# Optimization experiments

Measured on AMD Instinct MI355X. Metric: run time of the kernel, lower is better.

Reference implementation:

```python
import jax, jax.numpy as jnp
import numpy as np

N = 30000; F = 16; E = 300000
HD = 256; NH = 8; C = HD // NH; L = 3
S = 256; K = 128
NH_CA = 4; HDC = HD // NH_CA


def _ln(x, g, b):
    mu = jnp.mean(x, -1, keepdims=True)
    v = jnp.mean((x - mu) ** 2, -1, keepdims=True)
    return (x - mu) / jnp.sqrt(v + 1e-5) * g + b


def setup_inputs() -> dict:
    ks = iter(jax.random.split(jax.random.key(0), 64))
    def nrm(sh, s=0.05):
        return jax.random.normal(next(ks), sh, jnp.float32) * s
    def zeros(sh):
        return jnp.zeros(sh, jnp.float32)
    def ones(sh):
        return jnp.ones(sh, jnp.float32)
    inp = {}
    inp['x'] = jax.random.normal(next(ks), (N, F), jnp.float32)
    inp['edge_index'] = jax.random.randint(next(ks), (2, E), 0, N, jnp.int32)
    inp['batch'] = jnp.zeros((N,), jnp.int32)
    inp['sheet_node_idx'] = jax.random.randint(next(ks), (S, K), 0, N, jnp.int32)
    inp['sheet_features'] = jax.random.normal(next(ks), (S, F), jnp.float32)
    # pre_transform
    inp['pre_W'] = nrm((F, HD)); inp['pre_b'] = zeros((HD,))
    # stacked GATv2 layers (lin_l, lin_r, att, bias)
    inp['gat_Wl'] = nrm((L, HD, HD)); inp['gat_Wr'] = nrm((L, HD, HD))
    inp['gat_att'] = nrm((L, NH, C)); inp['gat_b'] = zeros((L, HD))
    # geometry encoder
    inp['geo_W1'] = nrm((F, HD)); inp['geo_b1'] = zeros((HD,))
    inp['geo_g1'] = ones((HD,)); inp['geo_be1'] = zeros((HD,))
    inp['geo_W2'] = nrm((HD, HD)); inp['geo_b2'] = zeros((HD,))
    inp['geo_g2'] = ones((HD,)); inp['geo_be2'] = zeros((HD,))
    # cross attention (4 heads)
    inp['ca_Wq'] = nrm((HD, HD)); inp['ca_bq'] = zeros((HD,))
    inp['ca_Wk'] = nrm((HD, HD)); inp['ca_bk'] = zeros((HD,))
    inp['ca_Wv'] = nrm((HD, HD)); inp['ca_bv'] = zeros((HD,))
    inp['ca_Wo'] = nrm((HD, HD)); inp['ca_bo'] = zeros((HD,))
    # q_mlp
    inp['q_W1'] = nrm((2 * HD, HD)); inp['q_b1'] = zeros((HD,))
    inp['q_g1'] = ones((HD,)); inp['q_be1'] = zeros((HD,))
    inp['q_W2'] = nrm((HD, HD // 2)); inp['q_b2'] = zeros((HD // 2,))
    inp['q_g2'] = ones((HD // 2,)); inp['q_be2'] = zeros((HD // 2,))
    inp['q_W3'] = nrm((HD // 2, 1)); inp['q_b3'] = zeros((1,))
    # state_done_predictor
    inp['d_W1'] = nrm((HD, HD // 2)); inp['d_b1'] = zeros((HD // 2,))
    inp['d_g1'] = ones((HD // 2,)); inp['d_be1'] = zeros((HD // 2,))
    inp['d_W2'] = nrm((HD // 2, 1)); inp['d_b2'] = zeros((1,))
    return inp


def _fwd(x, sheet_features, pre_W, pre_b, gat_Wl, gat_Wr, gat_att, gat_b,
         geo_W1, geo_b1, geo_g1, geo_be1, geo_W2, geo_b2, geo_g2, geo_be2,
         ca_Wq, ca_bq, ca_Wk, ca_bk, ca_Wv, ca_bv, ca_Wo, ca_bo,
         q_W1, q_b1, q_g1, q_be1, q_W2, q_b2, q_g2, q_be2, q_W3, q_b3,
         d_W1, d_b1, d_g1, d_be1, d_W2, d_b2,
         edge_index, batch, sheet_node_idx):
    loops = jnp.arange(N, dtype=edge_index.dtype)  # PyG GATv2Conv add_self_loops=True
    src = jnp.concatenate([edge_index[0], loops])
    dst = jnp.concatenate([edge_index[1], loops])
    h = x @ pre_W + pre_b  # [N, HD]
    for l in range(L):
        xl = (h @ gat_Wl[l]).reshape(N, NH, C)  # source messages
        xr = (h @ gat_Wr[l]).reshape(N, NH, C)  # target
        m = jax.nn.leaky_relu(xl[src] + xr[dst], 0.2)  # [E+N, NH, C]
        e = jnp.einsum('ehc,hc->eh', m, gat_att[l])
        emax = jax.ops.segment_max(e, dst, num_segments=N)
        a = jnp.exp(e - emax[dst])
        denom = jax.ops.segment_sum(a, dst, num_segments=N)
        alpha = a / (denom[dst] + 1e-16)  # scatter softmax over incoming edges
        h = jax.ops.segment_sum(alpha[:, :, None] * xl[src], dst, num_segments=N)
        h = jax.nn.elu(h.reshape(N, HD) + gat_b[l])
    cnt = jax.ops.segment_sum(jnp.ones((N,), h.dtype), batch, num_segments=1)
    g = jax.ops.segment_sum(h, batch, num_segments=1) / cnt[:, None]  # [1, HD]
    sheet = h[sheet_node_idx].mean(axis=1)  # [S, HD] per-sheet gather+mean
    geo = jax.nn.relu(_ln(sheet_features @ geo_W1 + geo_b1, geo_g1, geo_be1))
    geo = jax.nn.relu(_ln(geo @ geo_W2 + geo_b2, geo_g2, geo_be2))
    qh = (sheet @ ca_Wq + ca_bq).reshape(S, NH_CA, HDC)
    kh = (geo @ ca_Wk + ca_bk).reshape(S, NH_CA, HDC)
    vh = (geo @ ca_Wv + ca_bv).reshape(S, NH_CA, HDC)
    att = jax.nn.softmax(jnp.einsum('qhd,khd->hqk', qh, kh) / jnp.sqrt(jnp.float32(HDC)), axis=-1)
    fused = jnp.einsum('hqk,khd->qhd', att, vh).reshape(S, HD) @ ca_Wo + ca_bo
    hq = jnp.concatenate([fused, jnp.broadcast_to(g, (S, HD))], axis=1)  # [S, 2*HD]
    hq = jax.nn.relu(_ln(hq @ q_W1 + q_b1, q_g1, q_be1))
    hq = jax.nn.relu(_ln(hq @ q_W2 + q_b2, q_g2, q_be2))
    q_values = (hq @ q_W3 + q_b3)[:, 0]  # [S]
    hd = jax.nn.relu(_ln(g @ d_W1 + d_b1, d_g1, d_be1))
    done_logit = (hd @ d_W2 + d_b2)[:, 0]  # [1]
    return q_values, done_logit


def reference(x, edge_index, batch, sheet_node_idx, sheet_features, pre_W, pre_b,
              gat_Wl, gat_Wr, gat_att, gat_b,
              geo_W1, geo_b1, geo_g1, geo_be1, geo_W2, geo_b2, geo_g2, geo_be2,
              ca_Wq, ca_bq, ca_Wk, ca_bk, ca_Wv, ca_bv, ca_Wo, ca_bo,
              q_W1, q_b1, q_g1, q_be1, q_W2, q_b2, q_g2, q_be2, q_W3, q_b3,
              d_W1, d_b1, d_g1, d_be1, d_W2, d_b2):
    return _fwd(x, sheet_features, pre_W, pre_b, gat_Wl, gat_Wr, gat_att, gat_b,
                geo_W1, geo_b1, geo_g1, geo_be1, geo_W2, geo_b2, geo_g2, geo_be2,
                ca_Wq, ca_bq, ca_Wk, ca_bk, ca_Wv, ca_bv, ca_Wo, ca_bo,
                q_W1, q_b1, q_g1, q_be1, q_W2, q_b2, q_g2, q_be2, q_W3, q_b3,
                d_W1, d_b1, d_g1, d_be1, d_W2, d_b2,
                edge_index, batch, sheet_node_idx)
```

## Files before the change

### kernel.cpp

```cpp
#include <hip/hip_runtime.h>
#include <hip/hip_bf16.h>
#include <stdint.h>

#define NN 30000
#define MPAD 30080
#define FI 16
#define EE 300000
#define ETOT (EE + NN)
#define HD 256
#define NH 8
#define CH 32
#define NL 3
#define SS 256
#define KS 128
#define NHC 4
#define HC 64
#define GSB 256
#define RPB 118
#define SCB 118

typedef _Float16 half8 __attribute__((ext_vector_type(8)));
typedef _Float16 half4v __attribute__((ext_vector_type(4)));
typedef _Float16 half2v __attribute__((ext_vector_type(2)));
typedef float f32x4 __attribute__((ext_vector_type(4)));

__device__ __forceinline__ float wsum(float v) {
#pragma unroll
  for (int d = 1; d < 64; d <<= 1) v += __shfl_xor(v, d);
  return v;
}

__device__ __forceinline__ half2v h2max(half2v a, half2v b) {
#if __has_builtin(__builtin_elementwise_max)
  return __builtin_elementwise_max(a, b);
#else
  half2v r; r[0] = a[0] > b[0] ? a[0] : b[0]; r[1] = a[1] > b[1] ? a[1] : b[1];
  return r;
#endif
}

__device__ __forceinline__ float h2dot(half2v a, half2v b, float c) {
#if __has_builtin(__builtin_amdgcn_fdot2)
  return __builtin_amdgcn_fdot2(a, b, c, false);
#else
  return c + (float)a[0] * (float)b[0] + (float)a[1] * (float)b[1];
#endif
}

__device__ __forceinline__ float ln_fast(float a, int t, int n, float* red16,
    const float* __restrict__ G, const float* __restrict__ Be, bool relu)
{
  float av = (t < n) ? a : 0.f;
  float s = wsum(av), s2 = wsum(av * av);
  if ((t & 63) == 0) { red16[t >> 6] = s; red16[8 + (t >> 6)] = s2; }
  __syncthreads();
  float sum = red16[0] + red16[1] + red16[2] + red16[3];
  float sq  = red16[8] + red16[9] + red16[10] + red16[11];
  float mu = sum / n;
  float var = sq / n - mu * mu;
  float o = 0.f;
  if (t < n) {
    o = (a - mu) * rsqrtf(var + 1e-5f) * G[t] + Be[t];
    if (relu) o = fmaxf(o, 0.f);
  }
  __syncthreads();
  return o;
}

__global__ __launch_bounds__(256) void k_init(int* __restrict__ cnt,
    int* __restrict__ gcnt, _Float16* __restrict__ h16pad)
{
  int i = blockIdx.x * 256 + threadIdx.x;
  if (i < NN) cnt[i] = 0;
  if (i == 0) gcnt[0] = 0;
  if (i < (MPAD - NN) * HD) h16pad[i] = (_Float16)0.f;
}

__global__ __launch_bounds__(256) void k_wconv(const float* __restrict__ Wl,
    const float* __restrict__ Wr, _Float16* __restrict__ WT)
{
  int m = blockIdx.x >> 8;
  int n = blockIdx.x & 255;
  int k = threadIdx.x;
  int l = m >> 1;
  const float* W = (m & 1) ? (Wr + (size_t)l * HD * HD) : (Wl + (size_t)l * HD * HD);
  WT[((size_t)m * HD + n) * HD + k] = (_Float16)W[k * HD + n];
}

__global__ __launch_bounds__(256) void k_wconvT(
    const float* __restrict__ geo_W2, const float* __restrict__ ca_Wq,
    const float* __restrict__ ca_Wk, const float* __restrict__ ca_Wv,
    const float* __restrict__ ca_Wo, const float* __restrict__ q_W1,
    const float* __restrict__ q_W2,
    _Float16* __restrict__ Tgeo2, _Float16* __restrict__ Tq,
    _Float16* __restrict__ Tk, _Float16* __restrict__ Tv,
    _Float16* __restrict__ To, _Float16* __restrict__ Tq1,
    _Float16* __restrict__ Tq2)
{
  int b = blockIdx.x, t = threadIdx.x;
  if (b < 1280) {
    int seg = b >> 8;
    int n = b & 255;
    const float* src = (seg == 0) ? geo_W2 : (seg == 1) ? ca_Wq : (seg == 2) ? ca_Wk
                     : (seg == 3) ? ca_Wv : ca_Wo;
    _Float16* dst = (seg == 0) ? Tgeo2 : (seg == 1) ? Tq : (seg == 2) ? Tk
                  : (seg == 3) ? Tv : To;
    dst[(size_t)n * 256 + t] = (_Float16)src[(size_t)t * 256 + n];
  } else if (b < 1536) {
    int n = b - 1280;
    Tq1[(size_t)n * 512 + t]       = (_Float16)q_W1[(size_t)t * 256 + n];
    Tq1[(size_t)n * 512 + 256 + t] = (_Float16)q_W1[(size_t)(256 + t) * 256 + n];
  } else {
    int n = b - 1536;
    Tq2[(size_t)n * 256 + t] = (_Float16)q_W2[(size_t)t * 128 + n];
  }
}

__global__ __launch_bounds__(256) void k_pre(const float* __restrict__ x,
    const float* __restrict__ W, const float* __restrict__ b,
    _Float16* __restrict__ H16)
{
  __shared__ float Ws[FI][HD];
  __shared__ float xs[8][FI];
  int r0 = blockIdx.x * 8;
  int t = threadIdx.x;
  for (int i = t; i < FI * HD; i += 256) Ws[i >> 8][i & 255] = W[i];
  if (t < 8 * FI) xs[t >> 4][t & 15] = x[(size_t)(r0 + (t >> 4)) * FI + (t & 15)];
  __syncthreads();
  float bj = b[t];
  for (int r = 0; r < 8; ++r) {
    float acc = bj;
#pragma unroll
    for (int k = 0; k < FI; ++k) acc += xs[r][k] * Ws[k][t];
    H16[(size_t)(r0 + r) * HD + t] = (_Float16)acc;
  }
}

__global__ __launch_bounds__(256) void k_count(const int* __restrict__ ei, int* __restrict__ cnt)
{
  int i = blockIdx.x * 256 + threadIdx.x;
  if (i >= ETOT) return;
  int dst = (i < EE) ? ei[EE + i] : (i - EE);
  atomicAdd(&cnt[dst], 1);
}

__global__ __launch_bounds__(256) void k_scanA(const int* __restrict__ cnt,
    int* __restrict__ rowptr, int* __restrict__ btot)
{
  __shared__ int wt[4];
  int b = blockIdx.x, t = threadIdx.x;
  int i = b * 256 + t;
  int v = (i < NN) ? cnt[i] : 0;
  int lane = t & 63, w = t >> 6;
  int s = v;
#pragma unroll
  for (int d = 1; d < 64; d <<= 1) {
    int u = __shfl_up(s, d);
    if (lane >= d) s += u;
  }
  if (lane == 63) wt[w] = s;
  __syncthreads();
  int off = 0;
  for (int k = 0; k < w; ++k) off += wt[k];
  if (i < NN) rowptr[i] = off + s - v;
  if (t == 255) btot[b] = off + s;
}

__global__ __launch_bounds__(128) void k_scanB(const int* __restrict__ btot,
    int* __restrict__ boff, int* __restrict__ rowptr)
{
  __shared__ int wt[2];
  int t = threadIdx.x;
  int v = (t < SCB) ? btot[t] : 0;
  int lane = t & 63, w = t >> 6;
  int s = v;
#pragma unroll
  for (int d = 1; d < 64; d <<= 1) {
    int u = __shfl_up(s, d);
    if (lane >= d) s += u;
  }
  if (lane == 63) wt[w] = s;
  __syncthreads();
  int off = (w == 1) ? wt[0] : 0;
  if (t < SCB) boff[t] = off + s - v;
  if (t == 127) rowptr[NN] = wt[0] + wt[1];
}

__global__ __launch_bounds__(256) void k_scanC(int* __restrict__ rowptr,
    const int* __restrict__ boff, int* __restrict__ wptr)
{
  int b = blockIdx.x, t = threadIdx.x;
  int i = b * 256 + t;
  if (i < NN) {
    int r = rowptr[i] + boff[b];
    rowptr[i] = r;
    wptr[i] = r;
  }
}

__global__ __launch_bounds__(256) void k_scatter(const int* __restrict__ ei,
    int* __restrict__ wptr, int* __restrict__ csr_src)
{
  int i = blockIdx.x * 256 + threadIdx.x;
  if (i >= ETOT) return;
  int src = (i < EE) ? ei[i] : (i - EE);
  int dst = (i < EE) ? ei[EE + i] : (i - EE);
  int pos = atomicAdd(&wptr[dst], 1);
  csr_src[pos] = src;
}

#define BK 64
__global__ __launch_bounds__(256) void k_gemm16(const _Float16* __restrict__ A,
    const _Float16* __restrict__ WT,
    _Float16* __restrict__ Xl, _Float16* __restrict__ Xr)
{
  __shared__ __align__(16) _Float16 As[128 * BK];
  __shared__ __align__(16) _Float16 Bs[128 * BK];
  int t = threadIdx.x;
  int w = t >> 6, lane = t & 63;
  int row0 = blockIdx.x * 128;
  int ct = blockIdx.y;
  const _Float16* Bmat = WT + (size_t)(ct >> 1) * HD * HD + (size_t)(ct & 1) * 128 * HD;
  _Float16* Out = (ct >> 1) ? Xr : Xl;
  int j0 = (ct & 1) * 128;

  f32x4 acc[4][4] = {};
  int wr = w >> 1, wc = w & 1;

  for (int k0 = 0; k0 < HD; k0 += BK) {
#pragma unroll
    for (int i = 0; i < 4; ++i) {
      int p = (i * 4 + w) * 64 + lane;
      int row = p >> 3, s = p & 7;
      int g = s ^ (row & 7);
      const _Float16* srcA = A + (size_t)(row0 + row) * HD + k0 + g * 8;
      __builtin_amdgcn_global_load_lds(
        (const __attribute__((address_space(1))) void*)srcA,
        (__attribute__((address_space(3))) void*)((char*)As + (i * 4 + w) * 1024),
        16, 0, 0);
      const _Float16* srcB = Bmat + (size_t)row * HD + k0 + g * 8;
      __builtin_amdgcn_global_load_lds(
        (const __attribute__((address_space(1))) void*)srcB,
        (__attribute__((address_space(3))) void*)((char*)Bs + (i * 4 + w) * 1024),
        16, 0, 0);
    }
    __syncthreads();
#pragma unroll
    for (int ks = 0; ks < 2; ++ks) {
      half8 af[4], bfr[4];
      int kslot = ks * 4 + (lane >> 4);
#pragma unroll
      for (int mi = 0; mi < 4; ++mi) {
        int rl = wr * 64 + mi * 16 + (lane & 15);
        int ps = kslot ^ (rl & 7);
        af[mi] = *(const half8*)((const char*)As + rl * 128 + ps * 16);
      }
#pragma unroll
      for (int ni = 0; ni < 4; ++ni) {
        int nl = wc * 64 + ni * 16 + (lane & 15);
        int ps = kslot ^ (nl & 7);
        bfr[ni] = *(const half8*)((const char*)Bs + nl * 128 + ps * 16);
      }
#pragma unroll
      for (int mi = 0; mi < 4; ++mi)
#pragma unroll
        for (int ni = 0; ni < 4; ++ni)
          acc[mi][ni] = __builtin_amdgcn_mfma_f32_16x16x32_f16(af[mi], bfr[ni], acc[mi][ni], 0, 0, 0);
    }
    __syncthreads();
  }
  int crow = (lane >> 4) * 4;
  int ccol = lane & 15;
#pragma unroll
  for (int mi = 0; mi < 4; ++mi)
#pragma unroll
    for (int ni = 0; ni < 4; ++ni) {
      size_t base_r = row0 + wr * 64 + mi * 16 + crow;
      int c = j0 + wc * 64 + ni * 16 + ccol;
#pragma unroll
      for (int r = 0; r < 4; ++r)
        Out[(base_r + r) * HD + c] = (_Float16)acc[mi][ni][r];
    }
}

__global__ __launch_bounds__(256) void k_edgeagg(const _Float16* __restrict__ Xl,
    const _Float16* __restrict__ Xr, const float* __restrict__ attw,
    const float* __restrict__ bias, const int* __restrict__ rowptr,
    const int* __restrict__ csr_src, _Float16* __restrict__ H16)
{
  int node = blockIdx.x * 4 + (threadIdx.x >> 6);
  int lane = threadIdx.x & 63;
  if (node >= NN) return;
  int st = rowptr[node], en = rowptr[node + 1];
  int c = lane * 4;
  half4v xrv = *(const half4v*)(Xr + (size_t)node * HD + c);
  half2v r01; r01[0] = xrv[0]; r01[1] = xrv[1];
  half2v r23; r23[0] = xrv[2]; r23[1] = xrv[3];
  float4 wvf = *(const float4*)(attw + c);
  half2v w01; w01[0] = (_Float16)wvf.x; w01[1] = (_Float16)wvf.y;
  half2v w23; w23[0] = (_Float16)wvf.z; w23[1] = (_Float16)wvf.w;
  half2v c02; c02[0] = (_Float16)0.2f; c02[1] = (_Float16)0.2f;

  float mh = -1e30f, dsum = 0.f;
  float a0 = 0.f, a1 = 0.f, a2 = 0.f, a3 = 0.f;

  half4v vx[4];
#pragma unroll
  for (int k = 0; k < 4; ++k) {
    int ii = st + k; if (ii >= en) ii = en - 1;
    vx[k] = *(const half4v*)(Xl + (size_t)csr_src[ii] * HD + c);
  }

  for (int i = st; i < en; i += 4) {
    half4v nvx[4];
#pragma unroll
    for (int k = 0; k < 4; ++k) {
      int ii = i + 4 + k; ii = (ii < en) ? ii : (en - 1);
      nvx[k] = *(const half4v*)(Xl + (size_t)csr_src[ii] * HD + c);
    }
    float e[4];
#pragma unroll
    for (int k = 0; k < 4; ++k) {
      half2v x01; x01[0] = vx[k][0]; x01[1] = vx[k][1];
      half2v x23; x23[0] = vx[k][2]; x23[1] = vx[k][3];
      half2v s0 = x01 + r01;
      half2v s1 = x23 + r23;
      half2v m0 = h2max(s0, s0 * c02);
      half2v m1 = h2max(s1, s1 * c02);
      float ek = h2dot(m1, w23, h2dot(m0, w01, 0.f));
      ek += __shfl_xor(ek, 1);
      ek += __shfl_xor(ek, 2);
      ek += __shfl_xor(ek, 4);
      e[k] = (i + k < en) ? ek : -1e30f;
    }
    float pmax = fmaxf(fmaxf(e[0], e[1]), fmaxf(e[2], e[3]));
    if (__any(pmax > mh + 8.f)) {
      float nm = fmaxf(mh, pmax);
      float sc = __expf(mh - nm);
      a0 *= sc; a1 *= sc; a2 *= sc; a3 *= sc; dsum *= sc;
      mh = nm;
    }
    float ps = 0.f;
#pragma unroll
    for (int k = 0; k < 4; ++k) {
      float pw = __expf(e[k] - mh);
      a0 += pw * (float)vx[k][0];
      a1 += pw * (float)vx[k][1];
      a2 += pw * (float)vx[k][2];
      a3 += pw * (float)vx[k][3];
      ps += pw;
    }
    dsum += ps;
#pragma unroll
    for (int k = 0; k < 4; ++k) vx[k] = nvx[k];
  }
  float inv = 1.f / (dsum + 1e-16f);
  float4 bb = *(const float4*)(bias + c);
  float o0 = a0 * inv + bb.x, o1 = a1 * inv + bb.y;
  float o2 = a2 * inv + bb.z, o3 = a3 * inv + bb.w;
  o0 = (o0 > 0.f) ? o0 : expm1f(o0);
  o1 = (o1 > 0.f) ? o1 : expm1f(o1);
  o2 = (o2 > 0.f) ? o2 : expm1f(o2);
  o3 = (o3 > 0.f) ? o3 : expm1f(o3);
  half4v h4;
  h4[0] = (_Float16)o0; h4[1] = (_Float16)o1; h4[2] = (_Float16)o2; h4[3] = (_Float16)o3;
  *(half4v*)(H16 + (size_t)node * HD + c) = h4;
}

__global__ __launch_bounds__(256) void k_gsum(const _Float16* __restrict__ H,
    const int* __restrict__ batch, float* __restrict__ gpart, int* __restrict__ gcnt)
{
  __shared__ float flagf[RPB];
  __shared__ int scount;
  int b = blockIdx.x, t = threadIdx.x;
  int r0 = b * RPB;
  int nr = NN - r0; if (nr > RPB) nr = RPB; if (nr < 0) nr = 0;
  if (t == 0) scount = 0;
  __syncthreads();
  if (t < nr) {
    int ok = (batch[r0 + t] == 0) ? 1 : 0;
    flagf[t] = (float)ok;
    if (ok) atomicAdd(&scount, 1);
  }
  __syncthreads();
  float a0 = 0.f, a1 = 0.f, a2 = 0.f, a3 = 0.f;
  const _Float16* Hp = H + (size_t)r0 * HD + t;
  int r = 0;
  for (; r + 4 <= nr; r += 4) {
    float v0 = (float)Hp[(size_t)(r + 0) * HD];
    float v1 = (float)Hp[(size_t)(r + 1) * HD];
    float v2 = (float)Hp[(size_t)(r + 2) * HD];
    float v3 = (float)Hp[(size_t)(r + 3) * HD];
    a0 += v0 * flagf[r + 0]; a1 += v1 * flagf[r + 1];
    a2 += v2 * flagf[r + 2]; a3 += v3 * flagf[r + 3];
  }
  for (; r < nr; ++r) a0 += (float)Hp[(size_t)r * HD] * flagf[r];
  gpart[(size_t)b * HD + t] = (a0 + a1) + (a2 + a3);
  if (t == 0 && scount) atomicAdd(gcnt, scount);
}

__global__ __launch_bounds__(256) void k_gfin(const float* __restrict__ gpart,
    const int* __restrict__ gcnt, float* __restrict__ gvec)
{
  int t = threadIdx.x;
  float a0 = 0.f, a1 = 0.f, a2 = 0.f, a3 = 0.f;
  for (int b = 0; b < GSB; b += 4) {
    a0 += gpart[(size_t)b * HD + t];
    a1 += gpart[(size_t)(b + 1) * HD + t];
    a2 += gpart[(size_t)(b + 2) * HD + t];
    a3 += gpart[(size_t)(b + 3) * HD + t];
  }
  gvec[t] = ((a0 + a1) + (a2 + a3)) / (float)(*gcnt);
}

__global__ __launch_bounds__(256) void k_tail1(const _Float16* __restrict__ h16,
    const int* __restrict__ sheet_idx, const float* __restrict__ sheet_feat,
    const float* __restrict__ geo_W1, const float* __restrict__ geo_b1,
    const float* __restrict__ geo_g1, const float* __restrict__ geo_be1,
    _Float16* __restrict__ sh16, _Float16* __restrict__ g116)
{
  __shared__ float xf[FI];
  __shared__ int sidx[KS];
  __shared__ float red16[16];
  int s = blockIdx.x, t = threadIdx.x;

  if (t < KS) sidx[t] = sheet_idx[s * KS + t];
  if (t >= 240) xf[t - 240] = sheet_feat[s * FI + (t - 240)];
  __syncthreads();

  float pa[8] = {};
#pragma unroll 2
  for (int r = 0; r < KS; r += 8) {
#pragma unroll
    for (int u = 0; u < 8; ++u)
      pa[u] += (float)h16[(size_t)sidx[r + u] * HD + t];
  }
  float shv = ((pa[0] + pa[1]) + (pa[2] + pa[3]) + (pa[4] + pa[5]) + (pa[6] + pa[7])) * (1.f / KS);
  sh16[(size_t)s * HD + t] = (_Float16)shv;

  float a = geo_b1[t];
#pragma unroll
  for (int k = 0; k < FI; ++k) a += xf[k] * geo_W1[k * HD + t];
  float g1 = ln_fast(a, t, 256, red16, geo_g1, geo_be1, true);
  g116[(size_t)s * HD + t] = (_Float16)g1;
}

template <int KD, int NW>
__global__ __launch_bounds__(NW * 64) void k_stageLN(
    const _Float16* __restrict__ X, const _Float16* __restrict__ WT,
    const float* __restrict__ b, const float* __restrict__ G,
    const float* __restrict__ Be, _Float16* __restrict__ Y,
    const float* __restrict__ W3, const float* __restrict__ b3,
    float* __restrict__ outq)
{
  __shared__ float ps[NW * 16], ps2[NW * 16], pq[NW * 16];
  const int NCOL = NW * 64;
  int t = threadIdx.x;
  int w = t >> 6, lane = t & 63;
  int arow = lane & 15, kg = lane >> 4;
  int m0 = blockIdx.x * 16;
  int col0 = w * 64;

  f32x4 acc[4] = {};
#pragma unroll
  for (int ks = 0; ks < KD / 32; ++ks) {
    half8 af = *(const half8*)(X + (size_t)(m0 + arow) * KD + ks * 32 + kg * 8);
#pragma unroll
    for (int n = 0; n < 4; ++n) {
      half8 bf = *(const half8*)(WT + (size_t)(col0 + n * 16 + arow) * KD + ks * 32 + kg * 8);
      acc[n] = __builtin_amdgcn_mfma_f32_16x16x32_f16(af, bf, acc[n], 0, 0, 0);
    }
  }
#pragma unroll
  for (int n = 0; n < 4; ++n) {
    float bv = b[col0 + n * 16 + arow];
#pragma unroll
    for (int r = 0; r < 4; ++r) acc[n][r] += bv;
  }
  float s[4] = {}, s2[4] = {};
#pragma unroll
  for (int n = 0; n < 4; ++n)
#pragma unroll
    for (int r = 0; r < 4; ++r) { float v = acc[n][r]; s[r] += v; s2[r] += v * v; }
#pragma unroll
  for (int d = 1; d < 16; d <<= 1)
#pragma unroll
    for (int r = 0; r < 4; ++r) { s[r] += __shfl_xor(s[r], d); s2[r] += __shfl_xor(s2[r], d); }
  if (arow == 0) {
#pragma unroll
    for (int r = 0; r < 4; ++r) {
      ps[w * 16 + kg * 4 + r] = s[r];
      ps2[w * 16 + kg * 4 + r] = s2[r];
    }
  }
  __syncthreads();
  float mu[4], rs[4];
#pragma unroll
  for (int r = 0; r < 4; ++r) {
    float S = 0.f, S2 = 0.f;
#pragma unroll
    for (int w2 = 0; w2 < NW; ++w2) { S += ps[w2 * 16 + kg * 4 + r]; S2 += ps2[w2 * 16 + kg * 4 + r]; }
    float m = S / NCOL;
    float var = S2 / NCOL - m * m;
    mu[r] = m; rs[r] = rsqrtf(var + 1e-5f);
  }
#pragma unroll
  for (int n = 0; n < 4; ++n) {
    int col = col0 + n * 16 + arow;
    float gv = G[col], bev = Be[col];
#pragma unroll
    for (int r = 0; r < 4; ++r)
      acc[n][r] = fmaxf((acc[n][r] - mu[r]) * rs[r] * gv + bev, 0.f);
  }
  if (Y) {
#pragma unroll
    for (int n = 0; n < 4; ++n) {
      int col = col0 + n * 16 + arow;
#pragma unroll
      for (int r = 0; r < 4; ++r)
        Y[(size_t)(m0 + kg * 4 + r) * NCOL + col] = (_Float16)acc[n][r];
    }
  }
  if (outq) {
    float p[4] = {};
#pragma unroll
    for (int n = 0; n < 4; ++n) {
      float w3 = W3[col0 + n * 16 + arow];
#pragma unroll
      for (int r = 0; r < 4; ++r) p[r] += acc[n][r] * w3;
    }
#pragma unroll
    for (int d = 1; d < 16; d <<= 1)
#pragma unroll
      for (int r = 0; r < 4; ++r) p[r] += __shfl_xor(p[r], d);
    if (arow == 0)
#pragma unroll
      for (int r = 0; r < 4; ++r) pq[w * 16 + kg * 4 + r] = p[r];
    __syncthreads();
    if (w == 0 && arow == 0) {
#pragma unroll
      for (int r = 0; r < 4; ++r) {
        float o = b3[0];
#pragma unroll
        for (int w2 = 0; w2 < NW; ++w2) o += pq[w2 * 16 + kg * 4 + r];
        outq[m0 + kg * 4 + r] = o;
      }
    }
  }
}

__global__ __launch_bounds__(64) void k_qkv(
    const _Float16* __restrict__ sh16, const _Float16* __restrict__ g216,
    const _Float16* __restrict__ Tq, const _Float16* __restrict__ Tk,
    const _Float16* __restrict__ Tv,
    const float* __restrict__ bq, const float* __restrict__ bk,
    const float* __restrict__ bv,
    _Float16* __restrict__ qb, _Float16* __restrict__ kb, _Float16* __restrict__ vb)
{
  int lane = threadIdx.x;
  int arow = lane & 15, kg = lane >> 4;
  int m0 = blockIdx.x * 16;
  int col0 = blockIdx.y * 64;
  int mat = blockIdx.z;
  const _Float16* X = (mat == 0) ? sh16 : g216;
  const _Float16* WT = (mat == 0) ? Tq : (mat == 1) ? Tk : Tv;
  const float* b = (mat == 0) ? bq : (mat == 1) ? bk : bv;
  _Float16* Y = (mat == 0) ? qb : (mat == 1) ? kb : vb;

  f32x4 acc[4] = {};
#pragma unroll
  for (int ks = 0; ks < 8; ++ks) {
    half8 af = *(const half8*)(X + (size_t)(m0 + arow) * 256 + ks * 32 + kg * 8);
#pragma unroll
    for (int n = 0; n < 4; ++n) {
      half8 bf = *(const half8*)(WT + (size_t)(col0 + n * 16 + arow) * 256 + ks * 32 + kg * 8);
      acc[n] = __builtin_amdgcn_mfma_f32_16x16x32_f16(af, bf, acc[n], 0, 0, 0);
    }
  }
#pragma unroll
  for (int n = 0; n < 4; ++n) {
    int col = col0 + n * 16 + arow;
    float bv2 = b[col];
#pragma unroll
    for (int r = 0; r < 4; ++r)
      Y[(size_t)(m0 + kg * 4 + r) * 256 + col] = (_Float16)(acc[n][r] + bv2);
  }
}

__global__ __launch_bounds__(64) void k_wo(
    const _Float16* __restrict__ pv16, const _Float16* __restrict__ To,
    const float* __restrict__ bo, const float* __restrict__ gvec,
    _Float16* __restrict__ hqin)
{
  int lane = threadIdx.x;
  int arow = lane & 15, kg = lane >> 4;
  int m0 = blockIdx.x * 16;
  int col0 = blockIdx.y * 64;

  f32x4 acc[4] = {};
#pragma unroll
  for (int ks = 0; ks < 8; ++ks) {
    half8 af = *(const half8*)(pv16 + (size_t)(m0 + arow) * 256 + ks * 32 + kg * 8);
#pragma unroll
    for (int n = 0; n < 4; ++n) {
      half8 bf = *(const half8*)(To + (size_t)(col0 + n * 16 + arow) * 256 + ks * 32 + kg * 8);
      acc[n] = __builtin_amdgcn_mfma_f32_16x16x32_f16(af, bf, acc[n], 0, 0, 0);
    }
  }
#pragma unroll
  for (int n = 0; n < 4; ++n) {
    int col = col0 + n * 16 + arow;
    float bv = bo[col];
    _Float16 gg = (_Float16)gvec[col];
#pragma unroll
    for (int r = 0; r < 4; ++r) {
      hqin[(size_t)(m0 + kg * 4 + r) * 512 + col] = (_Float16)(acc[n][r] + bv);
      hqin[(size_t)(m0 + kg * 4 + r) * 512 + 256 + col] = gg;
    }
  }
}

__global__ __launch_bounds__(1024) void k_attn(const _Float16* __restrict__ qb,
    const _Float16* __restrict__ kb, const _Float16* __restrict__ vb,
    _Float16* __restrict__ pv16)
{
  __shared__ float qv[HD];
  __shared__ float att[1024];
  __shared__ float red4[1024];
  __shared__ float redm[16];
  __shared__ float reds[16];
  int row = blockIdx.x, t = threadIdx.x;
  int w = t >> 6;

  if (t < 256) qv[t] = (float)qb[(size_t)row * HD + t];
  __syncthreads();

  int h = t >> 8, key = t & 255;
  float e = 0.f;
  {
    const half8* kr = (const half8*)(kb + (size_t)key * HD + h * HC);
    const float* qh = qv + h * HC;
#pragma unroll
    for (int d = 0; d < 8; ++d) {
      half8 kk = kr[d];
#pragma unroll
      for (int u = 0; u < 8; ++u) e += qh[d * 8 + u] * (float)kk[u];
    }
    e *= 0.125f;
  }
  float wm = e;
#pragma unroll
  for (int d = 1; d < 64; d <<= 1) wm = fmaxf(wm, __shfl_xor(wm, d));
  if ((t & 63) == 0) redm[w] = wm;
  __syncthreads();
  float mx = fmaxf(fmaxf(redm[4 * h], redm[4 * h + 1]), fmaxf(redm[4 * h + 2], redm[4 * h + 3]));
  float pw = __expf(e - mx);
  float ws = wsum(pw);
  if ((t & 63) == 0) reds[w] = ws;
  att[t] = pw;
  __syncthreads();

  int kq = t >> 8, j = t & 255;
  int hj = j >> 6;
  float p = 0.f;
  const float* arow = att + hj * 256 + kq * 64;
  const _Float16* vcol = vb + (size_t)(kq * 64) * HD + j;
  for (int k = 0; k < 64; ++k)
    p += arow[k] * (float)vcol[(size_t)k * HD];
  red4[t] = p;
  __syncthreads();
  if (t < 256) {
    int hh = t >> 6;
    float dsum = reds[4 * hh] + reds[4 * hh + 1] + reds[4 * hh + 2] + reds[4 * hh + 3];
    float pv = (red4[t] + red4[256 + t] + red4[512 + t] + red4[768 + t]) / dsum;
    pv16[(size_t)row * HD + t] = (_Float16)pv;
  }
}

__global__ __launch_bounds__(256) void k_done(const float* __restrict__ gvec,
    const float* __restrict__ W1, const float* __restrict__ b1,
    const float* __restrict__ g1, const float* __restrict__ be1,
    const float* __restrict__ W2, const float* __restrict__ b2,
    float* __restrict__ out)
{
  __shared__ float gl[256];
  __shared__ float redc[256];
  __shared__ float red16[16];
  int t = threadIdx.x;
  gl[t] = gvec[t];
  __syncthreads();
  int j2 = t & 127, half = t >> 7;
  float p = 0.f;
#pragma unroll 8
  for (int k = half * 128; k < half * 128 + 128; ++k) p += gl[k] * W1[(size_t)k * 128 + j2];
  redc[t] = p;
  __syncthreads();
  float a = 0.f;
  if (t < 128) a = b1[t] + redc[t] + redc[128 + t];
  float hd = ln_fast(a, t, 128, red16, g1, be1, true);
  float vterm = (t < 128) ? hd * W2[t] : 0.f;
  float ss = wsum(vterm);
  if ((t & 63) == 0) red16[t >> 6] = ss;
  __syncthreads();
  if (t == 0) out[0] = red16[0] + red16[1] + red16[2] + red16[3] + b2[0];
}

extern "C" void kernel_launch(void* const* d_in, const int* in_sizes, int n_in,
                              void* d_out, int out_size, void* d_ws, size_t ws_size,
                              hipStream_t stream) {
  const float* x      = (const float*)d_in[0];
  const int*   ei     = (const int*)d_in[1];
  const int*   batch  = (const int*)d_in[2];
  const int*   sheet_idx = (const int*)d_in[3];
  const float* sheet_feat = (const float*)d_in[4];
  const float* pre_W  = (const float*)d_in[5];
  const float* pre_b  = (const float*)d_in[6];
  const float* gat_Wl = (const float*)d_in[7];
  const float* gat_Wr = (const float*)d_in[8];
  const float* gat_att = (const float*)d_in[9];
  const float* gat_b  = (const float*)d_in[10];
  const float* geo_W1 = (const float*)d_in[11];
  const float* geo_b1 = (const float*)d_in[12];
  const float* geo_g1 = (const float*)d_in[13];
  const float* geo_be1 = (const float*)d_in[14];
  const float* geo_W2 = (const float*)d_in[15];
  const float* geo_b2 = (const float*)d_in[16];
  const float* geo_g2 = (const float*)d_in[17];
  const float* geo_be2 = (const float*)d_in[18];
  const float* ca_Wq = (const float*)d_in[19];
  const float* ca_bq = (const float*)d_in[20];
  const float* ca_Wk = (const float*)d_in[21];
  const float* ca_bk = (const float*)d_in[22];
  const float* ca_Wv = (const float*)d_in[23];
  const float* ca_bv = (const float*)d_in[24];
  const float* ca_Wo = (const float*)d_in[25];
  const float* ca_bo = (const float*)d_in[26];
  const float* q_W1 = (const float*)d_in[27];
  const float* q_b1 = (const float*)d_in[28];
  const float* q_g1 = (const float*)d_in[29];
  const float* q_be1 = (const float*)d_in[30];
  const float* q_W2 = (const float*)d_in[31];
  const float* q_b2 = (const float*)d_in[32];
  const float* q_g2 = (const float*)d_in[33];
  const float* q_be2 = (const float*)d_in[34];
  const float* q_W3 = (const float*)d_in[35];
  const float* q_b3 = (const float*)d_in[36];
  const float* d_W1 = (const float*)d_in[37];
  const float* d_b1 = (const float*)d_in[38];
  const float* d_g1 = (const float*)d_in[39];
  const float* d_be1 = (const float*)d_in[40];
  const float* d_W2 = (const float*)d_in[41];
  const float* d_b2 = (const float*)d_in[42];

  char* wsb = (char*)d_ws;
  auto alloc = [&](size_t bytes) { char* p = wsb; wsb += (bytes + 255) & ~(size_t)255; return p; };

  _Float16* h16  = (_Float16*)alloc((size_t)MPAD * HD * 2);
  _Float16* Xl16 = (_Float16*)alloc((size_t)MPAD * HD * 2);
  _Float16* Xr16 = (_Float16*)alloc((size_t)MPAD * HD * 2);
  _Float16* WT   = (_Float16*)alloc((size_t)6 * HD * HD * 2);
  _Float16* Tgeo2 = (_Float16*)alloc((size_t)HD * HD * 2);
  _Float16* Tq   = (_Float16*)alloc((size_t)HD * HD * 2);
  _Float16* Tk   = (_Float16*)alloc((size_t)HD * HD * 2);
  _Float16* Tv   = (_Float16*)alloc((size_t)HD * HD * 2);
  _Float16* To   = (_Float16*)alloc((size_t)HD * HD * 2);
  _Float16* Tq1  = (_Float16*)alloc((size_t)HD * 512 * 2);
  _Float16* Tq2  = (_Float16*)alloc((size_t)128 * HD * 2);
  _Float16* sh16 = (_Float16*)alloc((size_t)SS * HD * 2);
  _Float16* g116 = (_Float16*)alloc((size_t)SS * HD * 2);
  _Float16* g216 = (_Float16*)alloc((size_t)SS * HD * 2);
  _Float16* qb16 = (_Float16*)alloc((size_t)SS * HD * 2);
  _Float16* kb16 = (_Float16*)alloc((size_t)SS * HD * 2);
  _Float16* vb16 = (_Float16*)alloc((size_t)SS * HD * 2);
  _Float16* pv16 = (_Float16*)alloc((size_t)SS * HD * 2);
  _Float16* hqin16 = (_Float16*)alloc((size_t)SS * 512 * 2);
  _Float16* hq116 = (_Float16*)alloc((size_t)SS * HD * 2);
  float* gpart   = (float*)alloc((size_t)GSB * HD * 4);
  float* gvec    = (float*)alloc(256 * 4);
  int* cnt       = (int*)alloc((size_t)NN * 4);
  int* rowptr    = (int*)alloc((size_t)(NN + 1) * 4);
  int* wptr      = (int*)alloc((size_t)NN * 4);
  int* csr_src   = (int*)alloc((size_t)ETOT * 4);
  int* btot      = (int*)alloc((size_t)SCB * 4);
  int* boff      = (int*)alloc((size_t)SCB * 4);
  int* gcnt      = (int*)alloc(4);

  float* out_q = (float*)d_out;
  float* out_d = out_q + SS;

  k_init<<<118, 256, 0, stream>>>(cnt, gcnt, h16 + (size_t)NN * HD);

  k_count<<<(ETOT + 255) / 256, 256, 0, stream>>>(ei, cnt);
  k_scanA<<<SCB, 256, 0, stream>>>(cnt, rowptr, btot);
  k_scanB<<<1, 128, 0, stream>>>(btot, boff, rowptr);
  k_scanC<<<SCB, 256, 0, stream>>>(rowptr, boff, wptr);
  k_scatter<<<(ETOT + 255) / 256, 256, 0, stream>>>(ei, wptr, csr_src);

  k_wconv<<<6 * 256, 256, 0, stream>>>(gat_Wl, gat_Wr, WT);
  k_wconvT<<<1664, 256, 0, stream>>>(geo_W2, ca_Wq, ca_Wk, ca_Wv, ca_Wo, q_W1, q_W2,
                                     Tgeo2, Tq, Tk, Tv, To, Tq1, Tq2);
  k_pre<<<NN / 8, 256, 0, stream>>>(x, pre_W, pre_b, h16);

  dim3 ggrid(MPAD / 128, 4);
  for (int l = 0; l < NL; ++l) {
    k_gemm16<<<ggrid, 256, 0, stream>>>(h16, WT + (size_t)l * 2 * HD * HD, Xl16, Xr16);
    k_edgeagg<<<(NN + 3) / 4, 256, 0, stream>>>(Xl16, Xr16, gat_att + l * NH * CH,
                                                gat_b + l * HD, rowptr, csr_src, h16);
  }

  k_gsum<<<GSB, 256, 0, stream>>>(h16, batch, gpart, gcnt);
  k_gfin<<<1, 256, 0, stream>>>(gpart, gcnt, gvec);

  k_tail1<<<SS, 256, 0, stream>>>(h16, sheet_idx, sheet_feat,
      geo_W1, geo_b1, geo_g1, geo_be1, sh16, g116);
  k_stageLN<256, 4><<<16, 256, 0, stream>>>(g116, Tgeo2, geo_b2, geo_g2, geo_be2,
      g216, nullptr, nullptr, nullptr);
  dim3 qkvg(16, 4, 3);
  k_qkv<<<qkvg, 64, 0, stream>>>(sh16, g216, Tq, Tk, Tv, ca_bq, ca_bk, ca_bv,
                                 qb16, kb16, vb16);
  k_attn<<<SS, 1024, 0, stream>>>(qb16, kb16, vb16, pv16);
  dim3 wog(16, 4);
  k_wo<<<wog, 64, 0, stream>>>(pv16, To, ca_bo, gvec, hqin16);
  k_stageLN<512, 4><<<16, 256, 0, stream>>>(hqin16, Tq1, q_b1, q_g1, q_be1,
      hq116, nullptr, nullptr, nullptr);
  k_stageLN<256, 2><<<16, 128, 0, stream>>>(hq116, Tq2, q_b2, q_g2, q_be2,
      nullptr, q_W3, q_b3, out_q);
  k_done<<<1, 256, 0, stream>>>(gvec, d_W1, d_b1, d_g1, d_be1, d_W2, d_b2, out_d);
}
```

Measured before the change: 323.3 us.

## Split edge aggregation across two half-waves and merge small launches

The GATv2 edge aggregation now gives each half of a wavefront its own edge stream, with 8 channels per lane. The two partial online softmaxes are merged with cross-half shuffles, which halves the serial edge loop per node at the cost of the merge step. Padding is added to the CSR array so the prefetch of a missing second edge stays in bounds. The weight conversion kernels are merged into one launch, and the global-mean finalisation and done-predictor kernels are folded as extra blocks into existing kernels to cut launch count.

```diff
diff --git a/kernel.cpp b/kernel.cpp
--- a/kernel.cpp
+++ b/kernel.cpp
@@ -30,6 +30,10 @@
   return v;
 }
 
+__device__ __forceinline__ half2v mk2(_Float16 a, _Float16 b) {
+  half2v r; r[0] = a; r[1] = b; return r;
+}
+
 __device__ __forceinline__ half2v h2max(half2v a, half2v b) {
 #if __has_builtin(__builtin_elementwise_max)
   return __builtin_elementwise_max(a, b);
@@ -68,36 +72,37 @@
 }
 
 __global__ __launch_bounds__(256) void k_init(int* __restrict__ cnt,
-    int* __restrict__ gcnt, _Float16* __restrict__ h16pad)
+    int* __restrict__ gcnt, _Float16* __restrict__ h16pad, int* __restrict__ csr_pad)
 {
   int i = blockIdx.x * 256 + threadIdx.x;
   if (i < NN) cnt[i] = 0;
   if (i == 0) gcnt[0] = 0;
+  if (i < 8) csr_pad[i] = 0;
   if (i < (MPAD - NN) * HD) h16pad[i] = (_Float16)0.f;
 }
 
-__global__ __launch_bounds__(256) void k_wconv(const float* __restrict__ Wl,
-    const float* __restrict__ Wr, _Float16* __restrict__ WT)
-{
-  int m = blockIdx.x >> 8;
-  int n = blockIdx.x & 255;
-  int k = threadIdx.x;
-  int l = m >> 1;
-  const float* W = (m & 1) ? (Wr + (size_t)l * HD * HD) : (Wl + (size_t)l * HD * HD);
-  WT[((size_t)m * HD + n) * HD + k] = (_Float16)W[k * HD + n];
-}
-
-__global__ __launch_bounds__(256) void k_wconvT(
+__global__ __launch_bounds__(256) void k_wconvAll(
+    const float* __restrict__ Wl, const float* __restrict__ Wr,
     const float* __restrict__ geo_W2, const float* __restrict__ ca_Wq,
     const float* __restrict__ ca_Wk, const float* __restrict__ ca_Wv,
     const float* __restrict__ ca_Wo, const float* __restrict__ q_W1,
     const float* __restrict__ q_W2,
+    _Float16* __restrict__ WT,
     _Float16* __restrict__ Tgeo2, _Float16* __restrict__ Tq,
     _Float16* __restrict__ Tk, _Float16* __restrict__ Tv,
     _Float16* __restrict__ To, _Float16* __restrict__ Tq1,
     _Float16* __restrict__ Tq2)
 {
   int b = blockIdx.x, t = threadIdx.x;
+  if (b < 1536) {
+    int m = b >> 8;
+    int n = b & 255;
+    int l = m >> 1;
+    const float* W = (m & 1) ? (Wr + (size_t)l * HD * HD) : (Wl + (size_t)l * HD * HD);
+    WT[((size_t)m * HD + n) * HD + t] = (_Float16)W[t * HD + n];
+    return;
+  }
+  b -= 1536;
   if (b < 1280) {
     int seg = b >> 8;
     int n = b & 255;
@@ -292,79 +297,83 @@
   int lane = threadIdx.x & 63;
   if (node >= NN) return;
   int st = rowptr[node], en = rowptr[node + 1];
-  int c = lane * 4;
-  half4v xrv = *(const half4v*)(Xr + (size_t)node * HD + c);
-  half2v r01; r01[0] = xrv[0]; r01[1] = xrv[1];
-  half2v r23; r23[0] = xrv[2]; r23[1] = xrv[3];
-  float4 wvf = *(const float4*)(attw + c);
-  half2v w01; w01[0] = (_Float16)wvf.x; w01[1] = (_Float16)wvf.y;
-  half2v w23; w23[0] = (_Float16)wvf.z; w23[1] = (_Float16)wvf.w;
-  half2v c02; c02[0] = (_Float16)0.2f; c02[1] = (_Float16)0.2f;
+  int n = en - st;
+  int hf = lane >> 5, sl = lane & 31;
+  int c = sl * 8;
+  half8 xrv = *(const half8*)(Xr + (size_t)node * HD + c);
+  float4 wa = *(const float4*)(attw + c);
+  float4 wb = *(const float4*)(attw + c + 4);
+  half2v w0 = mk2((_Float16)wa.x, (_Float16)wa.y);
+  half2v w1 = mk2((_Float16)wa.z, (_Float16)wa.w);
+  half2v w2 = mk2((_Float16)wb.x, (_Float16)wb.y);
+  half2v w3 = mk2((_Float16)wb.z, (_Float16)wb.w);
+  half2v r0 = mk2(xrv[0], xrv[1]), r1 = mk2(xrv[2], xrv[3]);
+  half2v r2 = mk2(xrv[4], xrv[5]), r3 = mk2(xrv[6], xrv[7]);
+  half2v c02 = mk2((_Float16)0.2f, (_Float16)0.2f);
 
   float mh = -1e30f, dsum = 0.f;
-  float a0 = 0.f, a1 = 0.f, a2 = 0.f, a3 = 0.f;
-
-  half4v vx[4];
-#pragma unroll
-  for (int k = 0; k < 4; ++k) {
-    int ii = st + k; if (ii >= en) ii = en - 1;
-    vx[k] = *(const half4v*)(Xl + (size_t)csr_src[ii] * HD + c);
-  }
-
-  for (int i = st; i < en; i += 4) {
-    half4v nvx[4];
-#pragma unroll
-    for (int k = 0; k < 4; ++k) {
-      int ii = i + 4 + k; ii = (ii < en) ? ii : (en - 1);
-      nvx[k] = *(const half4v*)(Xl + (size_t)csr_src[ii] * HD + c);
-    }
-    float e[4];
-#pragma unroll
-    for (int k = 0; k < 4; ++k) {
-      half2v x01; x01[0] = vx[k][0]; x01[1] = vx[k][1];
-      half2v x23; x23[0] = vx[k][2]; x23[1] = vx[k][3];
-      half2v s0 = x01 + r01;
-      half2v s1 = x23 + r23;
-      half2v m0 = h2max(s0, s0 * c02);
-      half2v m1 = h2max(s1, s1 * c02);
-      float ek = h2dot(m1, w23, h2dot(m0, w01, 0.f));
-      ek += __shfl_xor(ek, 1);
-      ek += __shfl_xor(ek, 2);
-      ek += __shfl_xor(ek, 4);
-      e[k] = (i + k < en) ? ek : -1e30f;
-    }
-    float pmax = fmaxf(fmaxf(e[0], e[1]), fmaxf(e[2], e[3]));
-    if (__any(pmax > mh + 8.f)) {
-      float nm = fmaxf(mh, pmax);
+  float a[8] = {};
+  int trips = (n + 1) >> 1;
+
+  int idx0 = csr_src[st + hf];
+  half8 xv = *(const half8*)(Xl + (size_t)idx0 * HD + c);
+
+  for (int it = 0; it < trips; ++it) {
+    bool valid = (2 * it + hf) < n;
+    half8 xc = xv;
+    if (it + 1 < trips) {
+      int nidx = csr_src[st + 2 * (it + 1) + hf];
+      xv = *(const half8*)(Xl + (size_t)nidx * HD + c);
+    }
+    half2v x0 = mk2(xc[0], xc[1]), x1 = mk2(xc[2], xc[3]);
+    half2v x2 = mk2(xc[4], xc[5]), x3 = mk2(xc[6], xc[7]);
+    half2v s0 = x0 + r0, s1 = x1 + r1, s2 = x2 + r2, s3 = x3 + r3;
+    half2v m0 = h2max(s0, s0 * c02);
+    half2v m1 = h2max(s1, s1 * c02);
+    half2v m2 = h2max(s2, s2 * c02);
+    half2v m3 = h2max(s3, s3 * c02);
+    float e = h2dot(m3, w3, h2dot(m2, w2, h2dot(m1, w1, h2dot(m0, w0, 0.f))));
+    e += __shfl_xor(e, 1);
+    e += __shfl_xor(e, 2);
+    e = valid ? e : -1e30f;
+    if (__any(e > mh + 8.f)) {
+      float nm = fmaxf(mh, e);
       float sc = __expf(mh - nm);
-      a0 *= sc; a1 *= sc; a2 *= sc; a3 *= sc; dsum *= sc;
+      dsum *= sc;
+#pragma unroll
+      for (int j = 0; j < 8; ++j) a[j] *= sc;
       mh = nm;
     }
-    float ps = 0.f;
-#pragma unroll
-    for (int k = 0; k < 4; ++k) {
-      float pw = __expf(e[k] - mh);
-      a0 += pw * (float)vx[k][0];
-      a1 += pw * (float)vx[k][1];
-      a2 += pw * (float)vx[k][2];
-      a3 += pw * (float)vx[k][3];
-      ps += pw;
-    }
-    dsum += ps;
-#pragma unroll
-    for (int k = 0; k < 4; ++k) vx[k] = nvx[k];
-  }
-  float inv = 1.f / (dsum + 1e-16f);
-  float4 bb = *(const float4*)(bias + c);
-  float o0 = a0 * inv + bb.x, o1 = a1 * inv + bb.y;
-  float o2 = a2 * inv + bb.z, o3 = a3 * inv + bb.w;
-  o0 = (o0 > 0.f) ? o0 : expm1f(o0);
-  o1 = (o1 > 0.f) ? o1 : expm1f(o1);
-  o2 = (o2 > 0.f) ? o2 : expm1f(o2);
-  o3 = (o3 > 0.f) ? o3 : expm1f(o3);
-  half4v h4;
-  h4[0] = (_Float16)o0; h4[1] = (_Float16)o1; h4[2] = (_Float16)o2; h4[3] = (_Float16)o3;
-  *(half4v*)(H16 + (size_t)node * HD + c) = h4;
+    float pw = valid ? __expf(e - mh) : 0.f;
+#pragma unroll
+    for (int j = 0; j < 8; ++j) a[j] += pw * (float)xc[j];
+    dsum += pw;
+  }
+  float om = __shfl_xor(mh, 32);
+  float od = __shfl_xor(dsum, 32);
+  float nm = fmaxf(mh, om);
+  float scs = __expf(mh - nm);
+  float sco = __expf(om - nm);
+  float d = dsum * scs + od * sco;
+#pragma unroll
+  for (int j = 0; j < 8; ++j) {
+    float oa = __shfl_xor(a[j], 32);
+    a[j] = a[j] * scs + oa * sco;
+  }
+  if (hf == 0) {
+    float inv = 1.f / (d + 1e-16f);
+    float4 ba = *(const float4*)(bias + c);
+    float4 bb = *(const float4*)(bias + c + 4);
+    float ob[8] = {ba.x, ba.y, ba.z, ba.w, bb.x, bb.y, bb.z, bb.w};
+    half8 h8;
+#pragma unroll
+    for (int j = 0; j < 8; ++j) {
+      float o = a[j] * inv + ob[j];
+      o = (o > 0.f) ? o : expm1f(o);
+      h8[j] = (_Float16)o;
+    }
+    *(half8*)(H16 + (size_t)node * HD + c) = h8;
+  }
 }
 
 __global__ __launch_bounds__(256) void k_gsum(const _Float16* __restrict__ H,
@@ -399,30 +408,30 @@
   if (t == 0 && scount) atomicAdd(gcnt, scount);
 }
 
-__global__ __launch_bounds__(256) void k_gfin(const float* __restrict__ gpart,
-    const int* __restrict__ gcnt, float* __restrict__ gvec)
-{
-  int t = threadIdx.x;
-  float a0 = 0.f, a1 = 0.f, a2 = 0.f, a3 = 0.f;
-  for (int b = 0; b < GSB; b += 4) {
-    a0 += gpart[(size_t)b * HD + t];
-    a1 += gpart[(size_t)(b + 1) * HD + t];
-    a2 += gpart[(size_t)(b + 2) * HD + t];
-    a3 += gpart[(size_t)(b + 3) * HD + t];
-  }
-  gvec[t] = ((a0 + a1) + (a2 + a3)) / (float)(*gcnt);
-}
-
 __global__ __launch_bounds__(256) void k_tail1(const _Float16* __restrict__ h16,
     const int* __restrict__ sheet_idx, const float* __restrict__ sheet_feat,
     const float* __restrict__ geo_W1, const float* __restrict__ geo_b1,
     const float* __restrict__ geo_g1, const float* __restrict__ geo_be1,
+    const float* __restrict__ gpart, const int* __restrict__ gcnt,
+    float* __restrict__ gvec,
     _Float16* __restrict__ sh16, _Float16* __restrict__ g116)
 {
   __shared__ float xf[FI];
   __shared__ int sidx[KS];
   __shared__ float red16[16];
   int s = blockIdx.x, t = threadIdx.x;
+
+  if (s == SS) {
+    float a0 = 0.f, a1 = 0.f, a2 = 0.f, a3 = 0.f;
+    for (int b = 0; b < GSB; b += 4) {
+      a0 += gpart[(size_t)b * HD + t];
+      a1 += gpart[(size_t)(b + 1) * HD + t];
+      a2 += gpart[(size_t)(b + 2) * HD + t];
+      a3 += gpart[(size_t)(b + 3) * HD + t];
+    }
+    gvec[t] = ((a0 + a1) + (a2 + a3)) / (float)(*gcnt);
+    return;
+  }
 
   if (t < KS) sidx[t] = sheet_idx[s * KS + t];
   if (t >= 240) xf[t - 240] = sheet_feat[s * FI + (t - 240)];
@@ -451,11 +460,34 @@
     const float* __restrict__ b, const float* __restrict__ G,
     const float* __restrict__ Be, _Float16* __restrict__ Y,
     const float* __restrict__ W3, const float* __restrict__ b3,
-    float* __restrict__ outq)
+    float* __restrict__ outq,
+    const float* __restrict__ gvec,
+    const float* __restrict__ dW1, const float* __restrict__ db1,
+    const float* __restrict__ dg1, const float* __restrict__ dbe1,
+    const float* __restrict__ dW2, const float* __restrict__ db2,
+    float* __restrict__ outd)
 {
   __shared__ float ps[NW * 16], ps2[NW * 16], pq[NW * 16];
   const int NCOL = NW * 64;
   int t = threadIdx.x;
+
+  if (outd != nullptr && blockIdx.x == 16) {
+    int w2 = t >> 6;
+    float acc2 = db1[t];
+    for (int k = 0; k < 256; ++k) acc2 += gvec[k] * dW1[(size_t)k * 128 + t];
+    float s = wsum(acc2), s2v = wsum(acc2 * acc2);
+    if ((t & 63) == 0) { ps[w2] = s; ps2[w2] = s2v; }
+    __syncthreads();
+    float S = ps[0] + ps[1], S2 = ps2[0] + ps2[1];
+    float mu = S * (1.f / 128.f), var = S2 * (1.f / 128.f) - mu * mu;
+    float hdv = fmaxf((acc2 - mu) * rsqrtf(var + 1e-5f) * dg1[t] + dbe1[t], 0.f);
+    float o = wsum(hdv * dW2[t]);
+    if ((t & 63) == 0) pq[w2] = o;
+    __syncthreads();
+    if (t == 0) outd[0] = pq[0] + pq[1] + db2[0];
+    return;
+  }
+
   int w = t >> 6, lane = t & 63;
   int arow = lane & 15, kg = lane >> 4;
   int m0 = blockIdx.x * 16;
@@ -675,34 +707,6 @@
     float pv = (red4[t] + red4[256 + t] + red4[512 + t] + red4[768 + t]) / dsum;
     pv16[(size_t)row * HD + t] = (_Float16)pv;
   }
-}
-
-__global__ __launch_bounds__(256) void k_done(const float* __restrict__ gvec,
-    const float* __restrict__ W1, const float* __restrict__ b1,
-    const float* __restrict__ g1, const float* __restrict__ be1,
-    const float* __restrict__ W2, const float* __restrict__ b2,
-    float* __restrict__ out)
-{
-  __shared__ float gl[256];
-  __shared__ float redc[256];
-  __shared__ float red16[16];
-  int t = threadIdx.x;
-  gl[t] = gvec[t];
-  __syncthreads();
-  int j2 = t & 127, half = t >> 7;
-  float p = 0.f;
-#pragma unroll 8
-  for (int k = half * 128; k < half * 128 + 128; ++k) p += gl[k] * W1[(size_t)k * 128 + j2];
-  redc[t] = p;
-  __syncthreads();
-  float a = 0.f;
-  if (t < 128) a = b1[t] + redc[t] + redc[128 + t];
-  float hd = ln_fast(a, t, 128, red16, g1, be1, true);
-  float vterm = (t < 128) ? hd * W2[t] : 0.f;
-  float ss = wsum(vterm);
-  if ((t & 63) == 0) red16[t >> 6] = ss;
-  __syncthreads();
-  if (t == 0) out[0] = red16[0] + red16[1] + red16[2] + red16[3] + b2[0];
 }
 
 extern "C" void kernel_launch(void* const* d_in, const int* in_sizes, int n_in,
@@ -780,7 +784,7 @@
   int* cnt       = (int*)alloc((size_t)NN * 4);
   int* rowptr    = (int*)alloc((size_t)(NN + 1) * 4);
   int* wptr      = (int*)alloc((size_t)NN * 4);
-  int* csr_src   = (int*)alloc((size_t)ETOT * 4);
+  int* csr_src   = (int*)alloc((size_t)(ETOT + 8) * 4);
   int* btot      = (int*)alloc((size_t)SCB * 4);
   int* boff      = (int*)alloc((size_t)SCB * 4);
   int* gcnt      = (int*)alloc(4);
@@ -788,7 +792,7 @@
   float* out_q = (float*)d_out;
   float* out_d = out_q + SS;
 
-  k_init<<<118, 256, 0, stream>>>(cnt, gcnt, h16 + (size_t)NN * HD);
+  k_init<<<118, 256, 0, stream>>>(cnt, gcnt, h16 + (size_t)NN * HD, csr_src + ETOT);
 
   k_count<<<(ETOT + 255) / 256, 256, 0, stream>>>(ei, cnt);
   k_scanA<<<SCB, 256, 0, stream>>>(cnt, rowptr, btot);
@@ -796,9 +800,9 @@
   k_scanC<<<SCB, 256, 0, stream>>>(rowptr, boff, wptr);
   k_scatter<<<(ETOT + 255) / 256, 256, 0, stream>>>(ei, wptr, csr_src);
 
-  k_wconv<<<6 * 256, 256, 0, stream>>>(gat_Wl, gat_Wr, WT);
-  k_wconvT<<<1664, 256, 0, stream>>>(geo_W2, ca_Wq, ca_Wk, ca_Wv, ca_Wo, q_W1, q_W2,
-                                     Tgeo2, Tq, Tk, Tv, To, Tq1, Tq2);
+  k_wconvAll<<<3200, 256, 0, stream>>>(gat_Wl, gat_Wr, geo_W2, ca_Wq, ca_Wk, ca_Wv,
+                                       ca_Wo, q_W1, q_W2,
+                                       WT, Tgeo2, Tq, Tk, Tv, To, Tq1, Tq2);
   k_pre<<<NN / 8, 256, 0, stream>>>(x, pre_W, pre_b, h16);
 
   dim3 ggrid(MPAD / 128, 4);
@@ -809,12 +813,12 @@
   }
 
   k_gsum<<<GSB, 256, 0, stream>>>(h16, batch, gpart, gcnt);
-  k_gfin<<<1, 256, 0, stream>>>(gpart, gcnt, gvec);
-
-  k_tail1<<<SS, 256, 0, stream>>>(h16, sheet_idx, sheet_feat,
-      geo_W1, geo_b1, geo_g1, geo_be1, sh16, g116);
+
+  k_tail1<<<SS + 1, 256, 0, stream>>>(h16, sheet_idx, sheet_feat,
+      geo_W1, geo_b1, geo_g1, geo_be1, gpart, gcnt, gvec, sh16, g116);
   k_stageLN<256, 4><<<16, 256, 0, stream>>>(g116, Tgeo2, geo_b2, geo_g2, geo_be2,
-      g216, nullptr, nullptr, nullptr);
+      g216, nullptr, nullptr, nullptr,
+      nullptr, nullptr, nullptr, nullptr, nullptr, nullptr, nullptr, nullptr);
   dim3 qkvg(16, 4, 3);
   k_qkv<<<qkvg, 64, 0, stream>>>(sh16, g216, Tq, Tk, Tv, ca_bq, ca_bk, ca_bv,
                                  qb16, kb16, vb16);
@@ -822,8 +826,9 @@
   dim3 wog(16, 4);
   k_wo<<<wog, 64, 0, stream>>>(pv16, To, ca_bo, gvec, hqin16);
   k_stageLN<512, 4><<<16, 256, 0, stream>>>(hqin16, Tq1, q_b1, q_g1, q_be1,
-      hq116, nullptr, nullptr, nullptr);
-  k_stageLN<256, 2><<<16, 128, 0, stream>>>(hq116, Tq2, q_b2, q_g2, q_be2,
-      nullptr, q_W3, q_b3, out_q);
-  k_done<<<1, 256, 0, stream>>>(gvec, d_W1, d_b1, d_g1, d_be1, d_W2, d_b2, out_d);
-}
+      hq116, nullptr, nullptr, nullptr,
+      nullptr, nullptr, nullptr, nullptr, nullptr, nullptr, nullptr, nullptr);
+  k_stageLN<256, 2><<<17, 128, 0, stream>>>(hq116, Tq2, q_b2, q_g2, q_be2,
+      nullptr, q_W3, q_b3, out_q,
+      gvec, d_W1, d_b1, d_g1, d_be1, d_W2, d_b2, out_d);
+}
```

After: 309.4 us. 4.3% less time.
